# Performance work log

Measured on AMD Instinct MI355X. Metric: run time of the kernel, lower is better.

Reference implementation:

```python
import jax, jax.numpy as jnp
import numpy as np

SEQ, BATCH, HID, OUT, NLAYERS = 2048, 16, 512, 10, 5


def setup_inputs() -> dict:
    key = jax.random.key(0)
    ks = jax.random.split(key, 5)
    scale_in = 1.0 / np.sqrt(HID)
    x = jax.random.normal(ks[0], (SEQ, BATCH, HID), dtype=jnp.float32)
    # Per-layer SRU weights: W maps input -> [x_tilde, f_gate, r_gate] (3H).
    Ws = jax.random.normal(ks[1], (NLAYERS, 3 * HID, HID), dtype=jnp.float32) * scale_in
    # Gate biases: [b_f, b_r] concatenated (2H per layer).
    bs = jax.random.normal(ks[2], (NLAYERS, 2 * HID), dtype=jnp.float32) * 0.1
    fc_W = jax.random.normal(ks[3], (OUT, HID), dtype=jnp.float32) * scale_in
    fc_b = jax.random.normal(ks[4], (OUT,), dtype=jnp.float32) * 0.1
    return {"x": x, "Ws": Ws, "bs": bs, "fc_W": fc_W, "fc_b": fc_b}


def _sru_layer(x, W, b):
    # x: [L, B, H]; W: [3H, H]; b: [2H]
    U = jnp.einsum("lbh,gh->lbg", x, W)  # [L, B, 3H]
    xt, zf, zr = jnp.split(U, 3, axis=-1)
    bf, br = jnp.split(b, 2)
    f = jax.nn.sigmoid(zf + bf)  # forget gate [L, B, H]
    r = jax.nn.sigmoid(zr + br)  # reset/highway gate

    def step(c_prev, inp):
        f_t, xt_t = inp
        c_t = f_t * c_prev + (1.0 - f_t) * xt_t
        return c_t, c_t

    c0 = jnp.zeros(x.shape[1:], dtype=x.dtype)
    _, c = jax.lax.scan(step, c0, (f, xt))  # c: [L, B, H]
    h = r * c + (1.0 - r) * x  # highway connection
    return h


def reference(x, Ws, bs, fc_W, fc_b):
    h = x
    for l in range(NLAYERS):
        h = _sru_layer(h, Ws[l], bs[l])
    out = jnp.einsum("lbh,oh->lbo", h, fc_W) + fc_b
    return out
```

## Files before the change

### kernel.cpp

```cpp
#include <hip/hip_runtime.h>
#include <hip/hip_bf16.h>

#define SEQ 2048
#define BATCH 16
#define HID 512
#define OUT_DIM 10
#define NLAYERS 5
#define M_ROWS (SEQ * BATCH)
#define N3H (3 * HID)
#define GK HID

#define CHUNK 32
#define NSEG (SEQ / CHUNK)

typedef __attribute__((ext_vector_type(8))) _Float16 f16x8;
typedef __attribute__((ext_vector_type(4))) float f32x4;
typedef __attribute__((ext_vector_type(8))) unsigned short u16x8;

__device__ __forceinline__ unsigned short f2h(float x) {
  return __builtin_bit_cast(unsigned short, (_Float16)x);
}
__device__ __forceinline__ float h2f(unsigned short v) {
  return (float)__builtin_bit_cast(_Float16, v);
}
__device__ __forceinline__ float sigm(float x) { return 1.f / (1.f + __expf(-x)); }

__global__ __launch_bounds__(256) void cvt_f32_to_f16(const float* __restrict__ in,
                                                      unsigned short* __restrict__ out) {
  size_t i = ((size_t)blockIdx.x * 256 + threadIdx.x) * 8;
  float4 a = *(const float4*)(in + i);
  float4 b = *(const float4*)(in + i + 4);
  u16x8 r;
  r[0] = f2h(a.x); r[1] = f2h(a.y); r[2] = f2h(a.z); r[3] = f2h(a.w);
  r[4] = f2h(b.x); r[5] = f2h(b.y); r[6] = f2h(b.z); r[7] = f2h(b.w);
  *(u16x8*)(out + i) = r;
}

__global__ __launch_bounds__(256) void gemm_mfma(const unsigned short* __restrict__ A,
                                                 const unsigned short* __restrict__ B,
                                                 unsigned short* __restrict__ C) {
  __shared__ unsigned short lds[3][8192];
  const int tid = threadIdx.x;
  const int nwg = (M_ROWS / 128) * (N3H / 128);
  const int cpx = nwg / 8;
  const int swz = (blockIdx.x % 8) * cpx + blockIdx.x / 8;
  const int bm = swz / (N3H / 128);
  const int bn = swz % (N3H / 128);
  const int lane = tid & 63;
  const int wid = tid >> 6;
  const int wm = (wid >> 1) * 64, wn = (wid & 1) * 64;

  const unsigned short* Ag = A + (size_t)bm * 128 * GK;
  const unsigned short* Bg = B + (size_t)bn * 128 * GK;

  const int s0 = tid, s1 = tid + 256;
  const int r0 = s0 >> 2, c0 = (s0 & 3) * 8;
  const int r1 = s1 >> 2, c1 = (s1 & 3) * 8;

  const int fr = lane & 15;
  const int ko = (lane >> 4) * 8;

  f32x4 acc[4][4];
#pragma unroll
  for (int i = 0; i < 4; ++i)
#pragma unroll
    for (int j = 0; j < 4; ++j) acc[i][j] = (f32x4){0.f, 0.f, 0.f, 0.f};

#define STAGE(buf, k0)                                                                              \
  {                                                                                                 \
    __builtin_amdgcn_global_load_lds(                                                               \
        (const __attribute__((address_space(1))) void*)(Ag + (size_t)r0 * GK + (k0) + c0),          \
        (__attribute__((address_space(3))) void*)&lds[buf][s0 * 8], 16, 0, 0);                      \
    __builtin_amdgcn_global_load_lds(                                                               \
        (const __attribute__((address_space(1))) void*)(Ag + (size_t)r1 * GK + (k0) + c1),          \
        (__attribute__((address_space(3))) void*)&lds[buf][s1 * 8], 16, 0, 0);                      \
    __builtin_amdgcn_global_load_lds(                                                               \
        (const __attribute__((address_space(1))) void*)(Bg + (size_t)r0 * GK + (k0) + c0),          \
        (__attribute__((address_space(3))) void*)&lds[buf][4096 + s0 * 8], 16, 0, 0);               \
    __builtin_amdgcn_global_load_lds(                                                               \
        (const __attribute__((address_space(1))) void*)(Bg + (size_t)r1 * GK + (k0) + c1),          \
        (__attribute__((address_space(3))) void*)&lds[buf][4096 + s1 * 8], 16, 0, 0);               \
  }

  STAGE(0, 0);
  STAGE(1, 32);
#pragma unroll 1
  for (int kt = 0; kt < 16; ++kt) {
    if (kt < 15) {
      asm volatile("s_waitcnt vmcnt(4)" ::: "memory");
    } else {
      asm volatile("s_waitcnt vmcnt(0)" ::: "memory");
    }
    __builtin_amdgcn_s_barrier();
    __builtin_amdgcn_sched_barrier(0);
    if (kt + 2 < 16) STAGE((kt + 2) % 3, (kt + 2) * 32);
    const int cb = kt % 3;
    f16x8 af[4], bfr[4];
#pragma unroll
    for (int t = 0; t < 4; ++t) {
      af[t]  = *(const f16x8*)&lds[cb][(wm + t * 16 + fr) * 32 + ko];
      bfr[t] = *(const f16x8*)&lds[cb][4096 + (wn + t * 16 + fr) * 32 + ko];
    }
#pragma unroll
    for (int mt = 0; mt < 4; ++mt)
#pragma unroll
      for (int nt = 0; nt < 4; ++nt)
        acc[mt][nt] = __builtin_amdgcn_mfma_f32_16x16x32_f16(af[mt], bfr[nt], acc[mt][nt], 0, 0, 0);
  }
#undef STAGE

  __syncthreads();
  unsigned short* cl = &lds[0][0];
  const int er = (lane >> 4) * 4;
#pragma unroll
  for (int mt = 0; mt < 4; ++mt)
#pragma unroll
    for (int nt = 0; nt < 4; ++nt) {
      const int row = wm + mt * 16 + er;
      const int col = wn + nt * 16 + fr;
#pragma unroll
      for (int j = 0; j < 4; ++j) cl[(row + j) * 136 + col] = f2h(acc[mt][nt][j]);
    }
  __syncthreads();
  unsigned short* Cb = C + (size_t)bm * 128 * N3H + bn * 128;
#pragma unroll
  for (int i = 0; i < 8; ++i) {
    int flat = i * 2048 + tid * 8;
    int r = flat >> 7, c = flat & 127;
    *(u16x8*)(Cb + (size_t)r * N3H + c) = *(const u16x8*)&cl[r * 136 + c];
  }
}

__global__ __launch_bounds__(256, 4) void sru_scan_fused(
    const unsigned short* __restrict__ U,
    const float* __restrict__ bias,
    unsigned long long* __restrict__ FC,
    unsigned short* hb) {
  const int s = blockIdx.x >> 4;
  const int b = blockIdx.x & 15;
  const int h0 = threadIdx.x << 1;
  const float bf0 = bias[h0], bf1 = bias[h0 + 1];
  const float br0 = bias[HID + h0], br1 = bias[HID + h0 + 1];

  const size_t rowstep = (size_t)BATCH * N3H;
  const unsigned short* Up = U + ((size_t)(s * CHUNK) * BATCH + b) * N3H + h0;

  unsigned fx0[CHUNK], fx1[CHUNK];
  float F0 = 1.f, F1 = 1.f, c0 = 0.f, c1 = 0.f;
#pragma unroll
  for (int i = 0; i < CHUNK; ++i) {
    const unsigned short* p = Up + (size_t)i * rowstep;
    unsigned xt = *(const unsigned*)(p);
    unsigned zf = *(const unsigned*)(p + HID);
    unsigned short fh0 = f2h(sigm(h2f((unsigned short)zf) + bf0));
    unsigned short fh1 = f2h(sigm(h2f((unsigned short)(zf >> 16)) + bf1));
    float f0 = h2f(fh0), f1 = h2f(fh1);
    c0 = f0 * c0 + (1.f - f0) * h2f((unsigned short)xt);
    c1 = f1 * c1 + (1.f - f1) * h2f((unsigned short)(xt >> 16));
    F0 *= f0; F1 *= f1;
    fx0[i] = (xt & 0xffffu) | ((unsigned)fh0 << 16);
    fx1[i] = (xt >> 16) | ((unsigned)fh1 << 16);
  }

  const size_t ch = ((size_t)s * BATCH + b) * HID + h0;
  atomicExch(&FC[ch],
             ((unsigned long long)__builtin_bit_cast(unsigned, c0) << 32) |
                 __builtin_bit_cast(unsigned, -F0));
  atomicExch(&FC[ch + 1],
             ((unsigned long long)__builtin_bit_cast(unsigned, c1) << 32) |
                 __builtin_bit_cast(unsigned, -F1));

  float ci0 = 0.f, ci1 = 0.f, P0 = 1.f, P1 = 1.f;
  for (int j = s - 1; j >= 0; --j) {
    const size_t cj = ((size_t)j * BATCH + b) * HID + h0;
    unsigned long long v0, v1;
    do { v0 = atomicAdd(&FC[cj], 0ULL); } while (!(v0 & 0x80000000ULL));
    do { v1 = atomicAdd(&FC[cj + 1], 0ULL); } while (!(v1 & 0x80000000ULL));
    float Fj0 = -__builtin_bit_cast(float, (unsigned)v0);
    float Cj0 = __builtin_bit_cast(float, (unsigned)(v0 >> 32));
    float Fj1 = -__builtin_bit_cast(float, (unsigned)v1);
    float Cj1 = __builtin_bit_cast(float, (unsigned)(v1 >> 32));
    ci0 += P0 * Cj0; P0 *= Fj0;
    ci1 += P1 * Cj1; P1 *= Fj1;
    if (P0 == 0.f && P1 == 0.f) break;
  }

  float cc0 = ci0, cc1 = ci1;
  const size_t hstep = (size_t)BATCH * HID;
  unsigned short* hp = hb + ((size_t)(s * CHUNK) * BATCH + b) * HID + h0;
#pragma unroll
  for (int i = 0; i < CHUNK; ++i) {
    unsigned zr = *(const unsigned*)(Up + (size_t)i * rowstep + 2 * HID);
    unsigned xv = *(const unsigned*)(hp + (size_t)i * hstep);
    float f0 = h2f((unsigned short)(fx0[i] >> 16));
    float f1 = h2f((unsigned short)(fx1[i] >> 16));
    cc0 = f0 * cc0 + (1.f - f0) * h2f((unsigned short)fx0[i]);
    cc1 = f1 * cc1 + (1.f - f1) * h2f((unsigned short)fx1[i]);
    float r0 = sigm(h2f((unsigned short)zr) + br0);
    float r1 = sigm(h2f((unsigned short)(zr >> 16)) + br1);
    float hn0 = r0 * cc0 + (1.f - r0) * h2f((unsigned short)xv);
    float hn1 = r1 * cc1 + (1.f - r1) * h2f((unsigned short)(xv >> 16));
    *(unsigned*)(hp + (size_t)i * hstep) = (unsigned)f2h(hn0) | ((unsigned)f2h(hn1) << 16);
  }
}

#define FCR 16
__global__ __launch_bounds__(256) void fc_kernel(const unsigned short* __restrict__ H,
                                                 const float* __restrict__ W,
                                                 const float* __restrict__ bv,
                                                 float* __restrict__ out) {
  __shared__ float hs[FCR][516];
  __shared__ float ws[OUT_DIM][516];
  const int tid = threadIdx.x;
  const size_t m0 = (size_t)blockIdx.x * FCR;
#pragma unroll
  for (int i = 0; i < 4; ++i) {
    int f = tid + i * 256;
    int row = f >> 6;
    int kq = f & 63;
    u16x8 v = *(const u16x8*)(H + (m0 + row) * 512 + kq * 8);
#pragma unroll
    for (int j = 0; j < 8; ++j) hs[row][kq * 8 + j] = h2f(v[j]);
  }
#pragma unroll
  for (int i = 0; i < 5; ++i) {
    int f = tid + i * 256;
    int row = f >> 7;
    int kq = f & 127;
    float4 v = *(const float4*)(W + row * 512 + kq * 4);
    *(float4*)&ws[row][kq * 4] = v;
  }
  __syncthreads();
  if (tid < FCR * OUT_DIM) {
    int row = tid / OUT_DIM;
    int o = tid - row * OUT_DIM;
    float acc = bv[o];
#pragma unroll 8
    for (int k = 0; k < 512; ++k) acc += hs[row][k] * ws[o][k];
    out[(m0 + row) * OUT_DIM + o] = acc;
  }
}

extern "C" void kernel_launch(void* const* d_in, const int* in_sizes, int n_in,
                              void* d_out, int out_size, void* d_ws, size_t ws_size,
                              hipStream_t stream) {
  const float* x   = (const float*)d_in[0];
  const float* Ws  = (const float*)d_in[1];
  const float* bs  = (const float*)d_in[2];
  const float* fcW = (const float*)d_in[3];
  const float* fcb = (const float*)d_in[4];
  float* out = (float*)d_out;

  char* ws = (char*)d_ws;
  const size_t MiB = 1024 * 1024;
  unsigned short* Ub = (unsigned short*)ws;
  unsigned short* hb = (unsigned short*)(ws + 96 * MiB);
  unsigned short* Wh = (unsigned short*)(ws + 128 * MiB);
  unsigned long long* FC = (unsigned long long*)(ws + 136 * MiB);

  hipMemsetAsync(FC, 0, (size_t)NLAYERS * NSEG * BATCH * HID * 8, stream);
  cvt_f32_to_f16<<<(NLAYERS * N3H * HID) / (256 * 8), 256, 0, stream>>>(Ws, Wh);
  cvt_f32_to_f16<<<(M_ROWS * HID) / (256 * 8), 256, 0, stream>>>(x, hb);

  for (int l = 0; l < NLAYERS; ++l) {
    gemm_mfma<<<(M_ROWS / 128) * (N3H / 128), 256, 0, stream>>>(
        hb, Wh + (size_t)l * N3H * HID, Ub);
    sru_scan_fused<<<NSEG * BATCH, 256, 0, stream>>>(
        Ub, bs + (size_t)l * 2 * HID,
        FC + (size_t)l * NSEG * BATCH * HID, hb);
  }
  fc_kernel<<<M_ROWS / FCR, 256, 0, stream>>>(hb, fcW, fcb, out);
}
```

Measured before the change: 628.7 us.

## Load GEMM weight fragments directly into registers, staging only activations in LDS

The GEMM no longer copies the weight (B) tile through shared memory. Each wave now loads its B fragments straight from global memory into ping-pong register sets, while the A tile keeps the triple-buffered global_load_lds pipeline. This shrinks LDS traffic and the LDS footprint per stage, and unrolls the k-loop by two to alternate the register buffers. In exchange, waves that share the same column block load the same weights redundantly. The compiler's own vmcnt waits on the register loads may also serialize the asynchronous LDS prefetches.

```diff
diff --git a/kernel.cpp b/kernel.cpp
--- a/kernel.cpp
+++ b/kernel.cpp
@@ -37,9 +37,9 @@
 }
 
 __global__ __launch_bounds__(256) void gemm_mfma(const unsigned short* __restrict__ A,
-                                                 const unsigned short* __restrict__ B,
+                                                 const unsigned short* __restrict__ W,
                                                  unsigned short* __restrict__ C) {
-  __shared__ unsigned short lds[3][8192];
+  __shared__ unsigned short lds[17408];
   const int tid = threadIdx.x;
   const int nwg = (M_ROWS / 128) * (N3H / 128);
   const int cpx = nwg / 8;
@@ -51,8 +51,6 @@
   const int wm = (wid >> 1) * 64, wn = (wid & 1) * 64;
 
   const unsigned short* Ag = A + (size_t)bm * 128 * GK;
-  const unsigned short* Bg = B + (size_t)bn * 128 * GK;
-
   const int s0 = tid, s1 = tid + 256;
   const int r0 = s0 >> 2, c0 = (s0 & 3) * 8;
   const int r1 = s1 >> 2, c1 = (s1 & 3) * 8;
@@ -60,57 +58,78 @@
   const int fr = lane & 15;
   const int ko = (lane >> 4) * 8;
 
+  const unsigned short* Wl = W + (size_t)(bn * 128 + wn + fr) * GK + ko;
+
   f32x4 acc[4][4];
 #pragma unroll
   for (int i = 0; i < 4; ++i)
 #pragma unroll
     for (int j = 0; j < 4; ++j) acc[i][j] = (f32x4){0.f, 0.f, 0.f, 0.f};
 
-#define STAGE(buf, k0)                                                                              \
+#define STAGE_A(buf, k0)                                                                            \
   {                                                                                                 \
     __builtin_amdgcn_global_load_lds(                                                               \
         (const __attribute__((address_space(1))) void*)(Ag + (size_t)r0 * GK + (k0) + c0),          \
-        (__attribute__((address_space(3))) void*)&lds[buf][s0 * 8], 16, 0, 0);                      \
+        (__attribute__((address_space(3))) void*)&lds[(buf) * 4096 + s0 * 8], 16, 0, 0);            \
     __builtin_amdgcn_global_load_lds(                                                               \
         (const __attribute__((address_space(1))) void*)(Ag + (size_t)r1 * GK + (k0) + c1),          \
-        (__attribute__((address_space(3))) void*)&lds[buf][s1 * 8], 16, 0, 0);                      \
-    __builtin_amdgcn_global_load_lds(                                                               \
-        (const __attribute__((address_space(1))) void*)(Bg + (size_t)r0 * GK + (k0) + c0),          \
-        (__attribute__((address_space(3))) void*)&lds[buf][4096 + s0 * 8], 16, 0, 0);               \
-    __builtin_amdgcn_global_load_lds(                                                               \
-        (const __attribute__((address_space(1))) void*)(Bg + (size_t)r1 * GK + (k0) + c1),          \
-        (__attribute__((address_space(3))) void*)&lds[buf][4096 + s1 * 8], 16, 0, 0);               \
-  }
-
-  STAGE(0, 0);
-  STAGE(1, 32);
+        (__attribute__((address_space(3))) void*)&lds[(buf) * 4096 + s1 * 8], 16, 0, 0);            \
+  }
+#define LOADB(dst, kk)                                                                              \
+  {                                                                                                 \
+    dst##0 = *(const f16x8*)(Wl + 0 * 16 * GK + (kk));                                              \
+    dst##1 = *(const f16x8*)(Wl + 1 * 16 * GK + (kk));                                              \
+    dst##2 = *(const f16x8*)(Wl + 2 * 16 * GK + (kk));                                              \
+    dst##3 = *(const f16x8*)(Wl + 3 * 16 * GK + (kk));                                              \
+  }
+#define DOMFMA(bv)                                                                                  \
+  {                                                                                                 \
+    f16x8 af[4];                                                                                    \
+    _Pragma("unroll") for (int t = 0; t < 4; ++t)                                                   \
+        af[t] = *(const f16x8*)&lds[abase + (wm + t * 16 + fr) * 32 + ko];                          \
+    _Pragma("unroll") for (int mt = 0; mt < 4; ++mt) {                                              \
+      acc[mt][0] = __builtin_amdgcn_mfma_f32_16x16x32_f16(af[mt], bv##0, acc[mt][0], 0, 0, 0);      \
+      acc[mt][1] = __builtin_amdgcn_mfma_f32_16x16x32_f16(af[mt], bv##1, acc[mt][1], 0, 0, 0);      \
+      acc[mt][2] = __builtin_amdgcn_mfma_f32_16x16x32_f16(af[mt], bv##2, acc[mt][2], 0, 0, 0);      \
+      acc[mt][3] = __builtin_amdgcn_mfma_f32_16x16x32_f16(af[mt], bv##3, acc[mt][3], 0, 0, 0);      \
+    }                                                                                               \
+  }
+
+  f16x8 brA0, brA1, brA2, brA3, brB0, brB1, brB2, brB3;
+  STAGE_A(0, 0);
+  STAGE_A(1, 32);
+  LOADB(brA, 0);
+
+  int buf = 0;
 #pragma unroll 1
-  for (int kt = 0; kt < 16; ++kt) {
-    if (kt < 15) {
-      asm volatile("s_waitcnt vmcnt(4)" ::: "memory");
-    } else {
-      asm volatile("s_waitcnt vmcnt(0)" ::: "memory");
-    }
+  for (int kt2 = 0; kt2 < 8; ++kt2) {
+    const int k0 = kt2 * 2;
+    asm volatile("s_waitcnt vmcnt(6)" ::: "memory");
     __builtin_amdgcn_s_barrier();
     __builtin_amdgcn_sched_barrier(0);
-    if (kt + 2 < 16) STAGE((kt + 2) % 3, (kt + 2) * 32);
-    const int cb = kt % 3;
-    f16x8 af[4], bfr[4];
-#pragma unroll
-    for (int t = 0; t < 4; ++t) {
-      af[t]  = *(const f16x8*)&lds[cb][(wm + t * 16 + fr) * 32 + ko];
-      bfr[t] = *(const f16x8*)&lds[cb][4096 + (wn + t * 16 + fr) * 32 + ko];
+    if (k0 + 2 < 16) STAGE_A((buf + 2) % 3, (k0 + 2) * 32);
+    LOADB(brB, (k0 + 1) * 32);
+    {
+      const int abase = buf * 4096;
+      DOMFMA(brA);
     }
-#pragma unroll
-    for (int mt = 0; mt < 4; ++mt)
-#pragma unroll
-      for (int nt = 0; nt < 4; ++nt)
-        acc[mt][nt] = __builtin_amdgcn_mfma_f32_16x16x32_f16(af[mt], bfr[nt], acc[mt][nt], 0, 0, 0);
-  }
-#undef STAGE
+    asm volatile("s_waitcnt vmcnt(6)" ::: "memory");
+    __builtin_amdgcn_s_barrier();
+    __builtin_amdgcn_sched_barrier(0);
+    if (k0 + 3 < 16) STAGE_A((buf + 3) % 3, (k0 + 3) * 32);
+    if (k0 + 2 < 16) LOADB(brA, (k0 + 2) * 32);
+    {
+      const int abase = ((buf + 1) % 3) * 4096;
+      DOMFMA(brB);
+    }
+    buf = (buf + 2) % 3;
+  }
+#undef STAGE_A
+#undef LOADB
+#undef DOMFMA
 
   __syncthreads();
-  unsigned short* cl = &lds[0][0];
+  unsigned short* cl = &lds[0];
   const int er = (lane >> 4) * 4;
 #pragma unroll
   for (int mt = 0; mt < 4; ++mt)
```

New measurement: 840.6 us. +33.7%, slower.
